# Kernel optimization log

Measured on AMD Instinct MI355X. Metric: run time of the kernel, lower is better.

## Reference

```python
import jax, jax.numpy as jnp
import numpy as np

H = 2048  # n_hidden
T = 2048  # sequence length
FUTURE = 128


def setup_inputs() -> dict:
    key = jax.random.key(0)
    ks = jax.random.split(key, 12)
    s = 1.0 / np.sqrt(H)  # torch default uniform init bound
    u = lambda k, shp: jax.random.uniform(k, shp, jnp.float32, -s, s)
    return {
        "input": jax.random.normal(ks[0], (T, 1), jnp.float32),
        "w_ih1": u(ks[1], (4 * H, 1)),
        "w_hh1": u(ks[2], (4 * H, H)),
        "b_ih1": u(ks[3], (4 * H,)),
        "b_hh1": u(ks[4], (4 * H,)),
        "w_ih2": u(ks[5], (4 * H, H)),
        "w_hh2": u(ks[6], (4 * H, H)),
        "b_ih2": u(ks[7], (4 * H,)),
        "b_hh2": u(ks[8], (4 * H,)),
        "w_lin": u(ks[9], (1, H)),
        "b_lin": u(ks[10], (1,)),
        "future": FUTURE,
    }


def _cell(x, h, c, w_ih, w_hh, b_ih, b_hh):
    # PyTorch LSTMCell: gates ordered (i, f, g, o)
    gates = x @ w_ih.T + b_ih + h @ w_hh.T + b_hh  # [1, 4H]
    i, f, g, o = jnp.split(gates, 4, axis=-1)
    c_new = jax.nn.sigmoid(f) * c + jax.nn.sigmoid(i) * jnp.tanh(g)
    h_new = jax.nn.sigmoid(o) * jnp.tanh(c_new)
    return h_new, c_new


def reference(input, w_ih1, w_hh1, b_ih1, b_hh1, w_ih2, w_hh2, b_ih2, b_hh2,
              w_lin, b_lin, future):
    zeros = jnp.zeros((1, H), jnp.float32)

    def step(carry, x):  # x: [1] -> [1,1]
        h1, c1, h2, c2 = carry
        h1, c1 = _cell(x[None, :], h1, c1, w_ih1, w_hh1, b_ih1, b_hh1)
        h2, c2 = _cell(h1, h2, c2, w_ih2, w_hh2, b_ih2, b_hh2)
        out = h2 @ w_lin.T + b_lin  # [1,1]
        return (h1, c1, h2, c2), out

    carry, ys = jax.lax.scan(step, (zeros, zeros, zeros, zeros), input)
    last_out = ys[-1]  # [1,1]

    def fstep(carry, _):
        h1, c1, h2, c2, out = carry
        h1, c1 = _cell(out, h1, c1, w_ih1, w_hh1, b_ih1, b_hh1)
        h2, c2 = _cell(h1, h2, c2, w_ih2, w_hh2, b_ih2, b_hh2)
        out = h2 @ w_lin.T + b_lin
        return (h1, c1, h2, c2, out), out

    _, ys_f = jax.lax.scan(fstep, (*carry, last_out), None, length=future)
    # concat along time, reshape to [1, T+future] (torch cats on dim=1)
    all_y = jnp.concatenate([ys, ys_f], axis=0)  # [T+future, 1, 1]
    return all_y.reshape(1, -1)
```

## Files before the change

kernel.cpp:

```cpp
#include <hip/hip_runtime.h>
#include <stdint.h>


typedef unsigned long long u64;
typedef unsigned int u32;

#define HD 2048
#define TT 2048
#define FUT 128
#define G4 8192

__device__ __forceinline__ float sigm_(float x) {
    return 1.0f / (1.0f + __expf(-x));
}
__device__ __forceinline__ float tanh_(float x) {
    float xc = fminf(fmaxf(x, -15.0f), 15.0f);
    float e = __expf(2.0f * xc);
    return 1.0f - 2.0f / (e + 1.0f);
}

__device__ __forceinline__ void poll2(u64* p0, u64* p1, u32 tag,
                                      float* o0, float* o1, int* alive) {
    u64 v0 = 0, v1 = 0;
    int d0 = 0, d1 = 0, guard = 0;
    while (*alive) {
        if (!d0) { v0 = __hip_atomic_load(p0, __ATOMIC_RELAXED, __HIP_MEMORY_SCOPE_AGENT); d0 = ((u32)(v0 >> 32) == tag); }
        if (!d1) { v1 = __hip_atomic_load(p1, __ATOMIC_RELAXED, __HIP_MEMORY_SCOPE_AGENT); d1 = ((u32)(v1 >> 32) == tag); }
        if (d0 & d1) break;
        __builtin_amdgcn_s_sleep(2);
        if (++guard > (1 << 21)) *alive = 0;
    }
    *o0 = __uint_as_float((u32)v0);
    *o1 = __uint_as_float((u32)v1);
}

__device__ __forceinline__ void publish1(u64* p, float v, u32 tag) {
    u64 pk = ((u64)tag << 32) | (u64)__float_as_uint(v);
    __hip_atomic_store(p, pk, __ATOMIC_RELAXED, __HIP_MEMORY_SCOPE_AGENT);
}

__global__ void __launch_bounds__(1024, 4)
recur_kernel(const float* __restrict__ Wrec,
             const float* __restrict__ aiv,
             const float* __restrict__ ba,
             const float* __restrict__ bb,
             const float* __restrict__ xseq,
             const float* __restrict__ ig2,
             u64* __restrict__ hex,
             float* __restrict__ hist,
             float* __restrict__ cfin)
{
    __shared__ float lds_h[HD];
    __shared__ float lds_p[32][33];
    __shared__ float lds_g[32];
    __shared__ float lds_x[TT];

    const int tid = threadIdx.x;
    const int br = tid & 31;
    const int chunk = tid >> 5;
    const int gate = br >> 3;
    const int jj = br & 7;
    const int row = gate * HD + blockIdx.x * 8 + jj;
    const int e0 = tid * 2, e1 = tid * 2 + 1;

    float w[64];
    {
        const float* src = Wrec + (size_t)row * HD + chunk * 64;
        #pragma unroll
        for (int q = 0; q < 64; q += 4) {
            float4 v = *reinterpret_cast<const float4*>(src + q);
            w[q] = v.x; w[q + 1] = v.y; w[q + 2] = v.z; w[q + 3] = v.w;
        }
    }
    const float myb = ba[row] + bb[row];
    const float myaiv = aiv ? aiv[row] : 0.0f;

    if (xseq) { lds_x[e0] = xseq[e0]; lds_x[e1] = xseq[e1]; }

    float c = 0.0f;
    int alive = 1;

    #pragma unroll 1
    for (int t = 0; t < TT; ++t) {
        if (t == 0) {
            lds_h[e0] = 0.0f; lds_h[e1] = 0.0f;
        } else {
            u64* src = hex + (size_t)((t - 1) & 1) * HD;
            poll2(src + e0, src + e1, (u32)t, &lds_h[e0], &lds_h[e1], &alive);
        }
        __syncthreads();

        float addv = 0.0f;
        if (tid < 32) addv = ig2 ? ig2[(size_t)t * G4 + row] : myaiv * lds_x[t];

        const float* hc = lds_h + chunk * 64;
        float a0 = 0, a1 = 0, a2 = 0, a3 = 0;
        #pragma unroll
        for (int q = 0; q < 64; q += 4) {
            a0 = fmaf(w[q + 0], hc[q + 0], a0);
            a1 = fmaf(w[q + 1], hc[q + 1], a1);
            a2 = fmaf(w[q + 2], hc[q + 2], a2);
            a3 = fmaf(w[q + 3], hc[q + 3], a3);
        }
        lds_p[chunk][br] = (a0 + a1) + (a2 + a3);
        __syncthreads();

        if (tid < 32) {
            float s0 = 0, s1 = 0, s2 = 0, s3 = 0;
            #pragma unroll
            for (int cc = 0; cc < 32; cc += 4) {
                s0 += lds_p[cc + 0][br];
                s1 += lds_p[cc + 1][br];
                s2 += lds_p[cc + 2][br];
                s3 += lds_p[cc + 3][br];
            }
            float gsum = (s0 + s1) + (s2 + s3) + myb + addv;
            lds_g[br] = (gate == 2) ? tanh_(gsum) : sigm_(gsum);
            if (br < 8) {
                float gi = lds_g[br], gf = lds_g[8 + br];
                float gg = lds_g[16 + br], go = lds_g[24 + br];
                c = gf * c + gi * gg;
                float h = go * tanh_(c);
                hist[(size_t)t * HD + blockIdx.x * 8 + br] = h;
                publish1(hex + (size_t)(t & 1) * HD + blockIdx.x * 8 + br, h, (u32)(t + 1));
            }
        }
    }
    if (tid < 8) cfin[blockIdx.x * 8 + tid] = c;
}

__global__ void __launch_bounds__(256)
ig2_gemm_kernel(const float* __restrict__ H1h, const float* __restrict__ W,
                float* __restrict__ IG2)
{
    __shared__ float As[16][132];
    __shared__ float Bs[16][132];
    const int tid = threadIdx.x;
    const int tx = tid & 15;
    const int ty = tid >> 4;
    const int r0 = blockIdx.x * 128;
    const int t0 = blockIdx.y * 128;
    const int stt = tid & 127;
    const int skc = tid >> 7;

    float acc[8][8];
    #pragma unroll
    for (int i = 0; i < 8; ++i)
        #pragma unroll
        for (int j = 0; j < 8; ++j) acc[i][j] = 0.0f;

    #pragma unroll 1
    for (int k0 = 0; k0 < HD; k0 += 16) {
        const float* pa = H1h + (size_t)(t0 + stt) * HD + k0 + skc * 8;
        const float* pb = W   + (size_t)(r0 + stt) * HD + k0 + skc * 8;
        float4 va0 = *reinterpret_cast<const float4*>(pa);
        float4 va1 = *reinterpret_cast<const float4*>(pa + 4);
        float4 vb0 = *reinterpret_cast<const float4*>(pb);
        float4 vb1 = *reinterpret_cast<const float4*>(pb + 4);
        __syncthreads();
        const int kb = skc * 8;
        As[kb + 0][stt] = va0.x; As[kb + 1][stt] = va0.y; As[kb + 2][stt] = va0.z; As[kb + 3][stt] = va0.w;
        As[kb + 4][stt] = va1.x; As[kb + 5][stt] = va1.y; As[kb + 6][stt] = va1.z; As[kb + 7][stt] = va1.w;
        Bs[kb + 0][stt] = vb0.x; Bs[kb + 1][stt] = vb0.y; Bs[kb + 2][stt] = vb0.z; Bs[kb + 3][stt] = vb0.w;
        Bs[kb + 4][stt] = vb1.x; Bs[kb + 5][stt] = vb1.y; Bs[kb + 6][stt] = vb1.z; Bs[kb + 7][stt] = vb1.w;
        __syncthreads();
        #pragma unroll
        for (int kk = 0; kk < 16; ++kk) {
            float4 fa0 = *reinterpret_cast<const float4*>(&As[kk][ty * 8]);
            float4 fa1 = *reinterpret_cast<const float4*>(&As[kk][ty * 8 + 4]);
            float4 fb0 = *reinterpret_cast<const float4*>(&Bs[kk][tx * 8]);
            float4 fb1 = *reinterpret_cast<const float4*>(&Bs[kk][tx * 8 + 4]);
            float av[8] = {fa0.x, fa0.y, fa0.z, fa0.w, fa1.x, fa1.y, fa1.z, fa1.w};
            float bv[8] = {fb0.x, fb0.y, fb0.z, fb0.w, fb1.x, fb1.y, fb1.z, fb1.w};
            #pragma unroll
            for (int i = 0; i < 8; ++i)
                #pragma unroll
                for (int j = 0; j < 8; ++j)
                    acc[i][j] = fmaf(av[i], bv[j], acc[i][j]);
        }
    }
    #pragma unroll
    for (int i = 0; i < 8; ++i) {
        float* pc = IG2 + (size_t)(t0 + ty * 8 + i) * G4 + (r0 + tx * 8);
        *reinterpret_cast<float4*>(pc)     = make_float4(acc[i][0], acc[i][1], acc[i][2], acc[i][3]);
        *reinterpret_cast<float4*>(pc + 4) = make_float4(acc[i][4], acc[i][5], acc[i][6], acc[i][7]);
    }
}

__global__ void __launch_bounds__(256)
outs_kernel(const float* __restrict__ H2h, const float* __restrict__ wl,
            const float* __restrict__ bl, float* __restrict__ out)
{
    const int t = blockIdx.x;
    const int tid = threadIdx.x;
    const float* h = H2h + (size_t)t * HD + tid * 8;
    const float* wp = wl + tid * 8;
    float4 h0 = *reinterpret_cast<const float4*>(h);
    float4 h1 = *reinterpret_cast<const float4*>(h + 4);
    float4 w0 = *reinterpret_cast<const float4*>(wp);
    float4 w1 = *reinterpret_cast<const float4*>(wp + 4);
    float s = h0.x * w0.x;
    s = fmaf(h0.y, w0.y, s); s = fmaf(h0.z, w0.z, s); s = fmaf(h0.w, w0.w, s);
    s = fmaf(h1.x, w1.x, s); s = fmaf(h1.y, w1.y, s);
    s = fmaf(h1.z, w1.z, s); s = fmaf(h1.w, w1.w, s);
    #pragma unroll
    for (int off = 32; off > 0; off >>= 1) s += __shfl_down(s, off, 64);
    __shared__ float red[4];
    if ((tid & 63) == 0) red[tid >> 6] = s;
    __syncthreads();
    if (tid == 0) out[t] = red[0] + red[1] + red[2] + red[3] + bl[0];
}

__global__ void __launch_bounds__(1024, 4)
future_kernel(const float* __restrict__ Whh1, const float* __restrict__ Wih2,
              const float* __restrict__ Whh2,
              const float* __restrict__ wih1,
              const float* __restrict__ bih1, const float* __restrict__ bhh1,
              const float* __restrict__ bih2, const float* __restrict__ bhh2,
              const float* __restrict__ wl, const float* __restrict__ bl,
              u64* __restrict__ h1ex, u64* __restrict__ h2ex,
              const float* __restrict__ c1f, const float* __restrict__ c2f,
              float* __restrict__ out)
{
    __shared__ float lds_h1[HD];
    __shared__ float lds_h2[HD];
    __shared__ float lds_wl[HD];
    __shared__ float lds_p[32][33];
    __shared__ float lds_g[32];
    __shared__ float lds_red[17];

    const int tid = threadIdx.x;
    const int rl = tid >> 5;
    const int kl = tid & 31;
    const int gate = rl >> 3, jj = rl & 7;
    const int row = gate * HD + blockIdx.x * 8 + jj;
    const int e0 = tid * 2, e1 = tid * 2 + 1;
    const int wid = tid >> 6;
    const int lane = tid & 63;

    float rb1 = 0, rb2 = 0, raiv = 0;
    if (tid < 32) {
        int rg = tid >> 3, rj = tid & 7;
        int rr = rg * HD + blockIdx.x * 8 + rj;
        rb1 = bih1[rr] + bhh1[rr];
        rb2 = bih2[rr] + bhh2[rr];
        raiv = wih1[rr];
    }
    const float blin = bl[0];
    lds_wl[e0] = wl[e0]; lds_wl[e1] = wl[e1];

    float c1 = 0.0f, c2 = 0.0f;
    if (tid < 8) {
        c1 = c1f[blockIdx.x * 8 + tid];
        c2 = c2f[blockIdx.x * 8 + tid];
    }
    int alive = 1;

    poll2(h1ex + HD + e0, h1ex + HD + e1, (u32)TT, &lds_h1[e0], &lds_h1[e1], &alive);

    #pragma unroll 1
    for (int t = TT; t < TT + FUT; ++t) {
        {
            u64* src = h2ex + (size_t)((t - 1) & 1) * HD;
            poll2(src + e0, src + e1, (u32)t, &lds_h2[e0], &lds_h2[e1], &alive);
        }
        __syncthreads();

        float s = fmaf(lds_wl[e0], lds_h2[e0], lds_wl[e1] * lds_h2[e1]);
        #pragma unroll
        for (int off = 32; off > 0; off >>= 1) s += __shfl_down(s, off, 64);
        if (lane == 0) lds_red[wid] = s;
        __syncthreads();
        float xcur;
        {
            float ss = 0;
            #pragma unroll
            for (int i2 = 0; i2 < 16; ++i2) ss += lds_red[i2];
            xcur = ss + blin;
        }
        if (t > TT && tid == 0 && blockIdx.x == 0) out[t - 1] = xcur;

        {
            const float* wr = Whh1 + (size_t)row * HD + kl * 4;
            const float* hb = lds_h1 + kl * 4;
            float a0 = 0, a1 = 0, a2 = 0, a3 = 0;
            #pragma unroll
            for (int q = 0; q < 16; ++q) {
                float4 wv = *reinterpret_cast<const float4*>(wr + q * 128);
                float4 hv = *reinterpret_cast<const float4*>(hb + q * 128);
                a0 = fmaf(wv.x, hv.x, a0); a1 = fmaf(wv.y, hv.y, a1);
                a2 = fmaf(wv.z, hv.z, a2); a3 = fmaf(wv.w, hv.w, a3);
            }
            lds_p[rl][kl] = (a0 + a1) + (a2 + a3);
        }
        __syncthreads();
        if (tid < 32) {
            float s0 = 0, s1 = 0, s2 = 0, s3 = 0;
            #pragma unroll
            for (int cc = 0; cc < 32; cc += 4) {
                s0 += lds_p[tid][cc + 0]; s1 += lds_p[tid][cc + 1];
                s2 += lds_p[tid][cc + 2]; s3 += lds_p[tid][cc + 3];
            }
            float g1 = (s0 + s1) + (s2 + s3) + rb1 + raiv * xcur;
            lds_g[tid] = ((tid >> 3) == 2) ? tanh_(g1) : sigm_(g1);
            if (tid < 8) {
                float gi = lds_g[tid], gf = lds_g[8 + tid];
                float gg = lds_g[16 + tid], go = lds_g[24 + tid];
                c1 = gf * c1 + gi * gg;
                float h = go * tanh_(c1);
                publish1(h1ex + (size_t)(t & 1) * HD + blockIdx.x * 8 + tid, h, (u32)(t + 1));
            }
        }
        {
            u64* src = h1ex + (size_t)(t & 1) * HD;
            poll2(src + e0, src + e1, (u32)(t + 1), &lds_h1[e0], &lds_h1[e1], &alive);
        }
        __syncthreads();

        {
            const float* wr1 = Wih2 + (size_t)row * HD + kl * 4;
            const float* wr2 = Whh2 + (size_t)row * HD + kl * 4;
            const float* hb1 = lds_h1 + kl * 4;
            const float* hb2 = lds_h2 + kl * 4;
            float a0 = 0, a1 = 0, a2 = 0, a3 = 0;
            #pragma unroll
            for (int q = 0; q < 16; ++q) {
                float4 wv = *reinterpret_cast<const float4*>(wr1 + q * 128);
                float4 hv = *reinterpret_cast<const float4*>(hb1 + q * 128);
                a0 = fmaf(wv.x, hv.x, a0); a1 = fmaf(wv.y, hv.y, a1);
                a2 = fmaf(wv.z, hv.z, a2); a3 = fmaf(wv.w, hv.w, a3);
            }
            #pragma unroll
            for (int q = 0; q < 16; ++q) {
                float4 wv = *reinterpret_cast<const float4*>(wr2 + q * 128);
                float4 hv = *reinterpret_cast<const float4*>(hb2 + q * 128);
                a0 = fmaf(wv.x, hv.x, a0); a1 = fmaf(wv.y, hv.y, a1);
                a2 = fmaf(wv.z, hv.z, a2); a3 = fmaf(wv.w, hv.w, a3);
            }
            lds_p[rl][kl] = (a0 + a1) + (a2 + a3);
        }
        __syncthreads();
        if (tid < 32) {
            float s0 = 0, s1 = 0, s2 = 0, s3 = 0;
            #pragma unroll
            for (int cc = 0; cc < 32; cc += 4) {
                s0 += lds_p[tid][cc + 0]; s1 += lds_p[tid][cc + 1];
                s2 += lds_p[tid][cc + 2]; s3 += lds_p[tid][cc + 3];
            }
            float g2 = (s0 + s1) + (s2 + s3) + rb2;
            lds_g[tid] = ((tid >> 3) == 2) ? tanh_(g2) : sigm_(g2);
            if (tid < 8) {
                float gi = lds_g[tid], gf = lds_g[8 + tid];
                float gg = lds_g[16 + tid], go = lds_g[24 + tid];
                c2 = gf * c2 + gi * gg;
                float h = go * tanh_(c2);
                publish1(h2ex + (size_t)(t & 1) * HD + blockIdx.x * 8 + tid, h, (u32)(t + 1));
            }
        }
    }

    {
        u64* src = h2ex + (size_t)((TT + FUT - 1) & 1) * HD;
        poll2(src + e0, src + e1, (u32)(TT + FUT), &lds_h2[e0], &lds_h2[e1], &alive);
    }
    __syncthreads();
    float s = fmaf(lds_wl[e0], lds_h2[e0], lds_wl[e1] * lds_h2[e1]);
    #pragma unroll
    for (int off = 32; off > 0; off >>= 1) s += __shfl_down(s, off, 64);
    if (lane == 0) lds_red[wid] = s;
    __syncthreads();
    if (tid == 0 && blockIdx.x == 0) {
        float ss = 0;
        #pragma unroll
        for (int i2 = 0; i2 < 16; ++i2) ss += lds_red[i2];
        out[TT + FUT - 1] = ss + blin;
    }
}


extern "C" void kernel_launch(void* const* d_in, const int* in_sizes, int n_in,
                              void* d_out, int out_size, void* d_ws, size_t ws_size,
                              hipStream_t stream) {
    const float* input = (const float*)d_in[0];
    const float* w_ih1 = (const float*)d_in[1];
    const float* w_hh1 = (const float*)d_in[2];
    const float* b_ih1 = (const float*)d_in[3];
    const float* b_hh1 = (const float*)d_in[4];
    const float* w_ih2 = (const float*)d_in[5];
    const float* w_hh2 = (const float*)d_in[6];
    const float* b_ih2 = (const float*)d_in[7];
    const float* b_hh2 = (const float*)d_in[8];
    const float* w_lin = (const float*)d_in[9];
    const float* b_lin = (const float*)d_in[10];
    float* out = (float*)d_out;

    char* ws = (char*)d_ws;
    u64*   h1ex = (u64*)(ws);
    u64*   h2ex = (u64*)(ws + 32768);
    float* H1   = (float*)(ws + 65536);
    float* H2   = (float*)(ws + 65536 + (size_t)16 * 1024 * 1024);
    float* IG2  = (float*)(ws + 65536 + (size_t)32 * 1024 * 1024);
    float* c1f  = (float*)(ws + 65536 + (size_t)96 * 1024 * 1024);
    float* c2f  = (float*)(ws + 65536 + (size_t)96 * 1024 * 1024 + 8192);

    {
        const float* Wrec = w_hh1; const float* aiv = w_ih1;
        const float* ba = b_ih1;   const float* bb = b_hh1;
        const float* xs = input;   const float* ig = nullptr;
        u64* hx = h1ex; float* hh = H1; float* cf = c1f;
        void* args[] = {&Wrec, &aiv, &ba, &bb, &xs, &ig, &hx, &hh, &cf};
        if (hipLaunchCooperativeKernel((const void*)recur_kernel, dim3(256), dim3(1024),
                                       args, 0, stream) != hipSuccess) {
            (void)hipGetLastError();
            hipLaunchKernelGGL(recur_kernel, dim3(256), dim3(1024), 0, stream,
                               Wrec, aiv, ba, bb, xs, ig, hx, hh, cf);
        }
    }

    hipLaunchKernelGGL(ig2_gemm_kernel, dim3(G4 / 128, TT / 128), dim3(256), 0, stream,
                       H1, w_ih2, IG2);

    {
        const float* Wrec = w_hh2; const float* aiv = nullptr;
        const float* ba = b_ih2;   const float* bb = b_hh2;
        const float* xs = nullptr; const float* ig = IG2;
        u64* hx = h2ex; float* hh = H2; float* cf = c2f;
        void* args[] = {&Wrec, &aiv, &ba, &bb, &xs, &ig, &hx, &hh, &cf};
        if (hipLaunchCooperativeKernel((const void*)recur_kernel, dim3(256), dim3(1024),
                                       args, 0, stream) != hipSuccess) {
            (void)hipGetLastError();
            hipLaunchKernelGGL(recur_kernel, dim3(256), dim3(1024), 0, stream,
                               Wrec, aiv, ba, bb, xs, ig, hx, hh, cf);
        }
    }

    hipLaunchKernelGGL(outs_kernel, dim3(TT), dim3(256), 0, stream, H2, w_lin, b_lin, out);

    {
        const float* a0 = w_hh1; const float* a1 = w_ih2; const float* a2 = w_hh2;
        const float* a3 = w_ih1;
        const float* a4 = b_ih1; const float* a5 = b_hh1;
        const float* a6 = b_ih2; const float* a7 = b_hh2;
        const float* a8 = w_lin; const float* a9 = b_lin;
        u64* a10 = h1ex; u64* a11 = h2ex;
        const float* a12 = c1f; const float* a13 = c2f;
        float* a14 = out;
        void* args[] = {&a0, &a1, &a2, &a3, &a4, &a5, &a6, &a7, &a8, &a9,
                        &a10, &a11, &a12, &a13, &a14};
        if (hipLaunchCooperativeKernel((const void*)future_kernel, dim3(256), dim3(1024),
                                       args, 0, stream) != hipSuccess) {
            (void)hipGetLastError();
            hipLaunchKernelGGL(future_kernel, dim3(256), dim3(1024), 0, stream,
                               a0, a1, a2, a3, a4, a5, a6, a7, a8, a9,
                               a10, a11, a12, a13, a14);
        }
    }
}
```

Before: 20.89 ms.

## Replace per-element tagged exchange with per-block flags and separate value buffers

Inter-block hidden-state exchange changes from polling 2048 tagged 64-bit words per step to polling 256 per-block u32 flags with one wavefront, then reading plain values after a barrier. Publishers write values relaxed and raise the block flag with a release store. Separately, the ig2 load is hoisted ahead of the poll, the recurrent weights live in float4 registers with vectorized LDS reads, and the IG2 GEMM now prefetches the next tile into registers. This cuts polling traffic but adds an extra barrier per step and depends on the flag release ordering the value stores correctly.

After: 28.83 ms. 38.0% more time.

```diff
diff --git a/kernel.cpp b/kernel.cpp
--- a/kernel.cpp
+++ b/kernel.cpp
@@ -10,6 +10,8 @@
 #define FUT 128
 #define G4 8192
 
+#define LD4(p) (*reinterpret_cast<const float4*>(p))
+
 __device__ __forceinline__ float sigm_(float x) {
     return 1.0f / (1.0f + __expf(-x));
 }
@@ -19,24 +21,24 @@
     return 1.0f - 2.0f / (e + 1.0f);
 }
 
-__device__ __forceinline__ void poll2(u64* p0, u64* p1, u32 tag,
-                                      float* o0, float* o1, int* alive) {
-    u64 v0 = 0, v1 = 0;
-    int d0 = 0, d1 = 0, guard = 0;
-    while (*alive) {
-        if (!d0) { v0 = __hip_atomic_load(p0, __ATOMIC_RELAXED, __HIP_MEMORY_SCOPE_AGENT); d0 = ((u32)(v0 >> 32) == tag); }
-        if (!d1) { v1 = __hip_atomic_load(p1, __ATOMIC_RELAXED, __HIP_MEMORY_SCOPE_AGENT); d1 = ((u32)(v1 >> 32) == tag); }
-        if (d0 & d1) break;
-        __builtin_amdgcn_s_sleep(2);
-        if (++guard > (1 << 21)) *alive = 0;
-    }
-    *o0 = __uint_as_float((u32)v0);
-    *o1 = __uint_as_float((u32)v1);
-}
-
-__device__ __forceinline__ void publish1(u64* p, float v, u32 tag) {
-    u64 pk = ((u64)tag << 32) | (u64)__float_as_uint(v);
-    __hip_atomic_store(p, pk, __ATOMIC_RELAXED, __HIP_MEMORY_SCOPE_AGENT);
+__device__ __forceinline__ void poll_flags(const u32* flags, u32 tag, int tid) {
+    if (tid < 64) {
+        const u64* f = (const u64*)flags;
+        int guard = 0;
+        for (;;) {
+            u64 a = __hip_atomic_load(f + tid,      __ATOMIC_RELAXED, __HIP_MEMORY_SCOPE_AGENT);
+            u64 b = __hip_atomic_load(f + 64 + tid, __ATOMIC_RELAXED, __HIP_MEMORY_SCOPE_AGENT);
+            int ok = ((u32)a >= tag) & ((u32)(a >> 32) >= tag) &
+                     ((u32)b >= tag) & ((u32)(b >> 32) >= tag);
+            if (__all(ok)) break;
+            __builtin_amdgcn_s_sleep(1);
+            if (++guard > (1 << 18)) break;
+        }
+    }
+}
+
+__global__ void init_flags_kernel(u32* p) {
+    p[blockIdx.x * 256 + threadIdx.x] = 0;
 }
 
 __global__ void __launch_bounds__(1024, 4)
@@ -46,7 +48,8 @@
              const float* __restrict__ bb,
              const float* __restrict__ xseq,
              const float* __restrict__ ig2,
-             u64* __restrict__ hex,
+             u32* __restrict__ flags,
+             u32* __restrict__ vals,
              float* __restrict__ hist,
              float* __restrict__ cfin)
 {
@@ -63,45 +66,48 @@
     const int row = gate * HD + blockIdx.x * 8 + jj;
     const int e0 = tid * 2, e1 = tid * 2 + 1;
 
-    float w[64];
-    {
-        const float* src = Wrec + (size_t)row * HD + chunk * 64;
-        #pragma unroll
-        for (int q = 0; q < 64; q += 4) {
-            float4 v = *reinterpret_cast<const float4*>(src + q);
-            w[q] = v.x; w[q + 1] = v.y; w[q + 2] = v.z; w[q + 3] = v.w;
-        }
-    }
+    const float* wsrc = Wrec + (size_t)row * HD + chunk * 64;
+    float4 w0 = LD4(wsrc +  0), w1 = LD4(wsrc +  4), w2  = LD4(wsrc +  8), w3  = LD4(wsrc + 12);
+    float4 w4 = LD4(wsrc + 16), w5 = LD4(wsrc + 20), w6  = LD4(wsrc + 24), w7  = LD4(wsrc + 28);
+    float4 w8 = LD4(wsrc + 32), w9 = LD4(wsrc + 36), w10 = LD4(wsrc + 40), w11 = LD4(wsrc + 44);
+    float4 w12 = LD4(wsrc + 48), w13 = LD4(wsrc + 52), w14 = LD4(wsrc + 56), w15 = LD4(wsrc + 60);
+
     const float myb = ba[row] + bb[row];
     const float myaiv = aiv ? aiv[row] : 0.0f;
 
     if (xseq) { lds_x[e0] = xseq[e0]; lds_x[e1] = xseq[e1]; }
 
     float c = 0.0f;
-    int alive = 1;
 
     #pragma unroll 1
     for (int t = 0; t < TT; ++t) {
+        float addv = 0.0f;
+        if (ig2 && tid < 32) addv = ig2[(size_t)t * G4 + row];
+
         if (t == 0) {
             lds_h[e0] = 0.0f; lds_h[e1] = 0.0f;
+            __syncthreads();
         } else {
-            u64* src = hex + (size_t)((t - 1) & 1) * HD;
-            poll2(src + e0, src + e1, (u32)t, &lds_h[e0], &lds_h[e1], &alive);
-        }
-        __syncthreads();
-
-        float addv = 0.0f;
-        if (tid < 32) addv = ig2 ? ig2[(size_t)t * G4 + row] : myaiv * lds_x[t];
+            poll_flags(flags, (u32)t, tid);
+            __syncthreads();
+            const u64* v64 = (const u64*)(vals + (size_t)((t - 1) & 1) * HD);
+            u64 v = __hip_atomic_load(v64 + tid, __ATOMIC_RELAXED, __HIP_MEMORY_SCOPE_AGENT);
+            lds_h[e0] = __uint_as_float((u32)v);
+            lds_h[e1] = __uint_as_float((u32)(v >> 32));
+            __syncthreads();
+        }
+        if (!ig2 && tid < 32) addv = myaiv * lds_x[t];
 
         const float* hc = lds_h + chunk * 64;
         float a0 = 0, a1 = 0, a2 = 0, a3 = 0;
-        #pragma unroll
-        for (int q = 0; q < 64; q += 4) {
-            a0 = fmaf(w[q + 0], hc[q + 0], a0);
-            a1 = fmaf(w[q + 1], hc[q + 1], a1);
-            a2 = fmaf(w[q + 2], hc[q + 2], a2);
-            a3 = fmaf(w[q + 3], hc[q + 3], a3);
-        }
+        #define ACC4(W, i) { float4 hv = LD4(hc + 4 * (i)); \
+            a0 = fmaf(W.x, hv.x, a0); a1 = fmaf(W.y, hv.y, a1); \
+            a2 = fmaf(W.z, hv.z, a2); a3 = fmaf(W.w, hv.w, a3); }
+        ACC4(w0, 0)  ACC4(w1, 1)  ACC4(w2, 2)   ACC4(w3, 3)
+        ACC4(w4, 4)  ACC4(w5, 5)  ACC4(w6, 6)   ACC4(w7, 7)
+        ACC4(w8, 8)  ACC4(w9, 9)  ACC4(w10, 10) ACC4(w11, 11)
+        ACC4(w12, 12) ACC4(w13, 13) ACC4(w14, 14) ACC4(w15, 15)
+        #undef ACC4
         lds_p[chunk][br] = (a0 + a1) + (a2 + a3);
         __syncthreads();
 
@@ -122,9 +128,13 @@
                 c = gf * c + gi * gg;
                 float h = go * tanh_(c);
                 hist[(size_t)t * HD + blockIdx.x * 8 + br] = h;
-                publish1(hex + (size_t)(t & 1) * HD + blockIdx.x * 8 + br, h, (u32)(t + 1));
-            }
-        }
+                __hip_atomic_store(vals + (size_t)(t & 1) * HD + blockIdx.x * 8 + br,
+                                   __float_as_uint(h), __ATOMIC_RELAXED, __HIP_MEMORY_SCOPE_AGENT);
+            }
+        }
+        if (tid == 0)
+            __hip_atomic_store(flags + blockIdx.x, (u32)(t + 1),
+                               __ATOMIC_RELEASE, __HIP_MEMORY_SCOPE_AGENT);
     }
     if (tid < 8) cfin[blockIdx.x * 8 + tid] = c;
 }
@@ -142,6 +152,7 @@
     const int t0 = blockIdx.y * 128;
     const int stt = tid & 127;
     const int skc = tid >> 7;
+    const int kb = skc * 8;
 
     float acc[8][8];
     #pragma unroll
@@ -149,27 +160,31 @@
         #pragma unroll
         for (int j = 0; j < 8; ++j) acc[i][j] = 0.0f;
 
+    const float* pa = H1h + (size_t)(t0 + stt) * HD + kb;
+    const float* pb = W   + (size_t)(r0 + stt) * HD + kb;
+    float4 va0 = LD4(pa), va1 = LD4(pa + 4);
+    float4 vb0 = LD4(pb), vb1 = LD4(pb + 4);
+    pa += 16; pb += 16;
+
     #pragma unroll 1
     for (int k0 = 0; k0 < HD; k0 += 16) {
-        const float* pa = H1h + (size_t)(t0 + stt) * HD + k0 + skc * 8;
-        const float* pb = W   + (size_t)(r0 + stt) * HD + k0 + skc * 8;
-        float4 va0 = *reinterpret_cast<const float4*>(pa);
-        float4 va1 = *reinterpret_cast<const float4*>(pa + 4);
-        float4 vb0 = *reinterpret_cast<const float4*>(pb);
-        float4 vb1 = *reinterpret_cast<const float4*>(pb + 4);
-        __syncthreads();
-        const int kb = skc * 8;
+        __syncthreads();
         As[kb + 0][stt] = va0.x; As[kb + 1][stt] = va0.y; As[kb + 2][stt] = va0.z; As[kb + 3][stt] = va0.w;
         As[kb + 4][stt] = va1.x; As[kb + 5][stt] = va1.y; As[kb + 6][stt] = va1.z; As[kb + 7][stt] = va1.w;
         Bs[kb + 0][stt] = vb0.x; Bs[kb + 1][stt] = vb0.y; Bs[kb + 2][stt] = vb0.z; Bs[kb + 3][stt] = vb0.w;
         Bs[kb + 4][stt] = vb1.x; Bs[kb + 5][stt] = vb1.y; Bs[kb + 6][stt] = vb1.z; Bs[kb + 7][stt] = vb1.w;
         __syncthreads();
+        if (k0 + 16 < HD) {
+            va0 = LD4(pa); va1 = LD4(pa + 4);
+            vb0 = LD4(pb); vb1 = LD4(pb + 4);
+            pa += 16; pb += 16;
+        }
         #pragma unroll
         for (int kk = 0; kk < 16; ++kk) {
-            float4 fa0 = *reinterpret_cast<const float4*>(&As[kk][ty * 8]);
-            float4 fa1 = *reinterpret_cast<const float4*>(&As[kk][ty * 8 + 4]);
-            float4 fb0 = *reinterpret_cast<const float4*>(&Bs[kk][tx * 8]);
-            float4 fb1 = *reinterpret_cast<const float4*>(&Bs[kk][tx * 8 + 4]);
+            float4 fa0 = LD4(&As[kk][ty * 8]);
+            float4 fa1 = LD4(&As[kk][ty * 8 + 4]);
+            float4 fb0 = LD4(&Bs[kk][tx * 8]);
+            float4 fb1 = LD4(&Bs[kk][tx * 8 + 4]);
             float av[8] = {fa0.x, fa0.y, fa0.z, fa0.w, fa1.x, fa1.y, fa1.z, fa1.w};
             float bv[8] = {fb0.x, fb0.y, fb0.z, fb0.w, fb1.x, fb1.y, fb1.z, fb1.w};
             #pragma unroll
@@ -195,10 +210,8 @@
     const int tid = threadIdx.x;
     const float* h = H2h + (size_t)t * HD + tid * 8;
     const float* wp = wl + tid * 8;
-    float4 h0 = *reinterpret_cast<const float4*>(h);
-    float4 h1 = *reinterpret_cast<const float4*>(h + 4);
-    float4 w0 = *reinterpret_cast<const float4*>(wp);
-    float4 w1 = *reinterpret_cast<const float4*>(wp + 4);
+    float4 h0 = LD4(h), h1 = LD4(h + 4);
+    float4 w0 = LD4(wp), w1 = LD4(wp + 4);
     float s = h0.x * w0.x;
     s = fmaf(h0.y, w0.y, s); s = fmaf(h0.z, w0.z, s); s = fmaf(h0.w, w0.w, s);
     s = fmaf(h1.x, w1.x, s); s = fmaf(h1.y, w1.y, s);
@@ -218,7 +231,8 @@
               const float* __restrict__ bih1, const float* __restrict__ bhh1,
               const float* __restrict__ bih2, const float* __restrict__ bhh2,
               const float* __restrict__ wl, const float* __restrict__ bl,
-              u64* __restrict__ h1ex, u64* __restrict__ h2ex,
+              u32* __restrict__ flags1, u32* __restrict__ vals1,
+              u32* __restrict__ flags2, u32* __restrict__ vals2,
               const float* __restrict__ c1f, const float* __restrict__ c2f,
               float* __restrict__ out)
 {
@@ -254,15 +268,25 @@
         c1 = c1f[blockIdx.x * 8 + tid];
         c2 = c2f[blockIdx.x * 8 + tid];
     }
-    int alive = 1;
-
-    poll2(h1ex + HD + e0, h1ex + HD + e1, (u32)TT, &lds_h1[e0], &lds_h1[e1], &alive);
+
+    poll_flags(flags1, (u32)TT, tid);
+    __syncthreads();
+    {
+        const u64* v64 = (const u64*)(vals1 + (size_t)((TT - 1) & 1) * HD);
+        u64 v = __hip_atomic_load(v64 + tid, __ATOMIC_RELAXED, __HIP_MEMORY_SCOPE_AGENT);
+        lds_h1[e0] = __uint_as_float((u32)v);
+        lds_h1[e1] = __uint_as_float((u32)(v >> 32));
+    }
 
     #pragma unroll 1
     for (int t = TT; t < TT + FUT; ++t) {
+        poll_flags(flags2, (u32)t, tid);
+        __syncthreads();
         {
-            u64* src = h2ex + (size_t)((t - 1) & 1) * HD;
-            poll2(src + e0, src + e1, (u32)t, &lds_h2[e0], &lds_h2[e1], &alive);
+            const u64* v64 = (const u64*)(vals2 + (size_t)((t - 1) & 1) * HD);
+            u64 v = __hip_atomic_load(v64 + tid, __ATOMIC_RELAXED, __HIP_MEMORY_SCOPE_AGENT);
+            lds_h2[e0] = __uint_as_float((u32)v);
+            lds_h2[e1] = __uint_as_float((u32)(v >> 32));
         }
         __syncthreads();
 
@@ -286,8 +310,8 @@
             float a0 = 0, a1 = 0, a2 = 0, a3 = 0;
             #pragma unroll
             for (int q = 0; q < 16; ++q) {
-                float4 wv = *reinterpret_cast<const float4*>(wr + q * 128);
-                float4 hv = *reinterpret_cast<const float4*>(hb + q * 128);
+                float4 wv = LD4(wr + q * 128);
+                float4 hv = LD4(hb + q * 128);
                 a0 = fmaf(wv.x, hv.x, a0); a1 = fmaf(wv.y, hv.y, a1);
                 a2 = fmaf(wv.z, hv.z, a2); a3 = fmaf(wv.w, hv.w, a3);
             }
@@ -308,12 +332,21 @@
                 float gg = lds_g[16 + tid], go = lds_g[24 + tid];
                 c1 = gf * c1 + gi * gg;
                 float h = go * tanh_(c1);
-                publish1(h1ex + (size_t)(t & 1) * HD + blockIdx.x * 8 + tid, h, (u32)(t + 1));
-            }
-        }
+                __hip_atomic_store(vals1 + (size_t)(t & 1) * HD + blockIdx.x * 8 + tid,
+                                   __float_as_uint(h), __ATOMIC_RELAXED, __HIP_MEMORY_SCOPE_AGENT);
+            }
+        }
+        if (tid == 0)
+            __hip_atomic_store(flags1 + blockIdx.x, (u32)(t + 1),
+                               __ATOMIC_RELEASE, __HIP_MEMORY_SCOPE_AGENT);
+
+        poll_flags(flags1, (u32)(t + 1), tid);
+        __syncthreads();
         {
-            u64* src = h1ex + (size_t)(t & 1) * HD;
-            poll2(src + e0, src + e1, (u32)(t + 1), &lds_h1[e0], &lds_h1[e1], &alive);
+            const u64* v64 = (const u64*)(vals1 + (size_t)(t & 1) * HD);
+            u64 v = __hip_atomic_load(v64 + tid, __ATOMIC_RELAXED, __HIP_MEMORY_SCOPE_AGENT);
+            lds_h1[e0] = __uint_as_float((u32)v);
+            lds_h1[e1] = __uint_as_float((u32)(v >> 32));
         }
         __syncthreads();
 
@@ -325,15 +358,15 @@
             float a0 = 0, a1 = 0, a2 = 0, a3 = 0;
             #pragma unroll
             for (int q = 0; q < 16; ++q) {
-                float4 wv = *reinterpret_cast<const float4*>(wr1 + q * 128);
-                float4 hv = *reinterpret_cast<const float4*>(hb1 + q * 128);
+                float4 wv = LD4(wr1 + q * 128);
+                float4 hv = LD4(hb1 + q * 128);
                 a0 = fmaf(wv.x, hv.x, a0); a1 = fmaf(wv.y, hv.y, a1);
                 a2 = fmaf(wv.z, hv.z, a2); a3 = fmaf(wv.w, hv.w, a3);
             }
             #pragma unroll
             for (int q = 0; q < 16; ++q) {
-                float4 wv = *reinterpret_cast<const float4*>(wr2 + q * 128);
-                float4 hv = *reinterpret_cast<const float4*>(hb2 + q * 128);
+                float4 wv = LD4(wr2 + q * 128);
+                float4 hv = LD4(hb2 + q * 128);
                 a0 = fmaf(wv.x, hv.x, a0); a1 = fmaf(wv.y, hv.y, a1);
                 a2 = fmaf(wv.z, hv.z, a2); a3 = fmaf(wv.w, hv.w, a3);
             }
@@ -354,14 +387,22 @@
                 float gg = lds_g[16 + tid], go = lds_g[24 + tid];
                 c2 = gf * c2 + gi * gg;
                 float h = go * tanh_(c2);
-                publish1(h2ex + (size_t)(t & 1) * HD + blockIdx.x * 8 + tid, h, (u32)(t + 1));
-            }
-        }
-    }
-
+                __hip_atomic_store(vals2 + (size_t)(t & 1) * HD + blockIdx.x * 8 + tid,
+                                   __float_as_uint(h), __ATOMIC_RELAXED, __HIP_MEMORY_SCOPE_AGENT);
+            }
+        }
+        if (tid == 0)
+            __hip_atomic_store(flags2 + blockIdx.x, (u32)(t + 1),
+                               __ATOMIC_RELEASE, __HIP_MEMORY_SCOPE_AGENT);
+    }
+
+    poll_flags(flags2, (u32)(TT + FUT), tid);
+    __syncthreads();
     {
-        u64* src = h2ex + (size_t)((TT + FUT - 1) & 1) * HD;
-        poll2(src + e0, src + e1, (u32)(TT + FUT), &lds_h2[e0], &lds_h2[e1], &alive);
+        const u64* v64 = (const u64*)(vals2 + (size_t)((TT + FUT - 1) & 1) * HD);
+        u64 v = __hip_atomic_load(v64 + tid, __ATOMIC_RELAXED, __HIP_MEMORY_SCOPE_AGENT);
+        lds_h2[e0] = __uint_as_float((u32)v);
+        lds_h2[e1] = __uint_as_float((u32)(v >> 32));
     }
     __syncthreads();
     float s = fmaf(lds_wl[e0], lds_h2[e0], lds_wl[e1] * lds_h2[e1]);
@@ -395,25 +436,29 @@
     float* out = (float*)d_out;
 
     char* ws = (char*)d_ws;
-    u64*   h1ex = (u64*)(ws);
-    u64*   h2ex = (u64*)(ws + 32768);
+    u32*   flags1 = (u32*)(ws);
+    u32*   flags2 = (u32*)(ws + 4096);
+    u32*   vals1  = (u32*)(ws + 8192);
+    u32*   vals2  = (u32*)(ws + 32768);
     float* H1   = (float*)(ws + 65536);
     float* H2   = (float*)(ws + 65536 + (size_t)16 * 1024 * 1024);
     float* IG2  = (float*)(ws + 65536 + (size_t)32 * 1024 * 1024);
     float* c1f  = (float*)(ws + 65536 + (size_t)96 * 1024 * 1024);
     float* c2f  = (float*)(ws + 65536 + (size_t)96 * 1024 * 1024 + 8192);
 
+    hipLaunchKernelGGL(init_flags_kernel, dim3(8), dim3(256), 0, stream, (u32*)ws);
+
     {
         const float* Wrec = w_hh1; const float* aiv = w_ih1;
         const float* ba = b_ih1;   const float* bb = b_hh1;
         const float* xs = input;   const float* ig = nullptr;
-        u64* hx = h1ex; float* hh = H1; float* cf = c1f;
-        void* args[] = {&Wrec, &aiv, &ba, &bb, &xs, &ig, &hx, &hh, &cf};
+        u32* fl = flags1; u32* vl = vals1; float* hh = H1; float* cf = c1f;
+        void* args[] = {&Wrec, &aiv, &ba, &bb, &xs, &ig, &fl, &vl, &hh, &cf};
         if (hipLaunchCooperativeKernel((const void*)recur_kernel, dim3(256), dim3(1024),
                                        args, 0, stream) != hipSuccess) {
             (void)hipGetLastError();
             hipLaunchKernelGGL(recur_kernel, dim3(256), dim3(1024), 0, stream,
-                               Wrec, aiv, ba, bb, xs, ig, hx, hh, cf);
+                               Wrec, aiv, ba, bb, xs, ig, fl, vl, hh, cf);
         }
     }
 
@@ -424,13 +469,13 @@
         const float* Wrec = w_hh2; const float* aiv = nullptr;
         const float* ba = b_ih2;   const float* bb = b_hh2;
         const float* xs = nullptr; const float* ig = IG2;
-        u64* hx = h2ex; float* hh = H2; float* cf = c2f;
-        void* args[] = {&Wrec, &aiv, &ba, &bb, &xs, &ig, &hx, &hh, &cf};
+        u32* fl = flags2; u32* vl = vals2; float* hh = H2; float* cf = c2f;
+        void* args[] = {&Wrec, &aiv, &ba, &bb, &xs, &ig, &fl, &vl, &hh, &cf};
         if (hipLaunchCooperativeKernel((const void*)recur_kernel, dim3(256), dim3(1024),
                                        args, 0, stream) != hipSuccess) {
             (void)hipGetLastError();
             hipLaunchKernelGGL(recur_kernel, dim3(256), dim3(1024), 0, stream,
-                               Wrec, aiv, ba, bb, xs, ig, hx, hh, cf);
+                               Wrec, aiv, ba, bb, xs, ig, fl, vl, hh, cf);
         }
     }
 
@@ -442,17 +487,17 @@
         const float* a4 = b_ih1; const float* a5 = b_hh1;
         const float* a6 = b_ih2; const float* a7 = b_hh2;
         const float* a8 = w_lin; const float* a9 = b_lin;
-        u64* a10 = h1ex; u64* a11 = h2ex;
+        u32* f1 = flags1; u32* v1 = vals1; u32* f2 = flags2; u32* v2 = vals2;
         const float* a12 = c1f; const float* a13 = c2f;
         float* a14 = out;
         void* args[] = {&a0, &a1, &a2, &a3, &a4, &a5, &a6, &a7, &a8, &a9,
-                        &a10, &a11, &a12, &a13, &a14};
+                        &f1, &v1, &f2, &v2, &a12, &a13, &a14};
         if (hipLaunchCooperativeKernel((const void*)future_kernel, dim3(256), dim3(1024),
                                        args, 0, stream) != hipSuccess) {
             (void)hipGetLastError();
             hipLaunchKernelGGL(future_kernel, dim3(256), dim3(1024), 0, stream,
                                a0, a1, a2, a3, a4, a5, a6, a7, a8, a9,
-                               a10, a11, a12, a13, a14);
-        }
-    }
-}
+                               f1, v1, f2, v2, a12, a13, a14);
+        }
+    }
+}
```
